# Kernel optimization log

Hardware: AMD Instinct MI355X
Metric: run time of the kernel (lower is better)

## Reference

```python
import jax, jax.numpy as jnp
import numpy as np
from jax import lax

H, W = 8192, 8192
KH, KW = 3, 3


def setup_inputs() -> dict:
    key = jax.random.key(0)
    k1, k2 = jax.random.split(key)
    x = jax.random.normal(k1, (H, W), dtype=jnp.float32)
    weight = jax.random.uniform(k2, (KH, KW), dtype=jnp.float32)
    bias = jnp.zeros((1,), dtype=jnp.float32)
    return {"x": x, "weight": weight, "bias": bias}


def reference(x, weight, bias):
    # Valid 2D cross-correlation (same math as the nested-loop corr2d) + scalar bias.
    # x: [H, W], weight: [kh, kw] -> out: [H-kh+1, W-kw+1]
    out = lax.conv_general_dilated(
        x[None, None, :, :],           # NCHW
        weight[None, None, :, :],      # OIHW
        window_strides=(1, 1),
        padding="VALID",
    )[0, 0]
    return out + bias[0]
```

## Files before the change

### kernel.cpp

```cpp
#include <hip/hip_runtime.h>


static constexpr int H  = 8192;
static constexpr int W  = 8192;
static constexpr int OH = H - 2;
static constexpr int OW = W - 2;

typedef float f32x4 __attribute__((ext_vector_type(4)));
typedef float f32x2 __attribute__((ext_vector_type(2)));

__global__ __launch_bounds__(256) void conv3x3_kernel(
    const float* __restrict__ x,
    const float* __restrict__ w,
    const float* __restrict__ bias,
    float* __restrict__ out)
{
    const int c = (blockIdx.x * 64 + (int)threadIdx.x) * 8;
    const int r = (blockIdx.y * 4 + (int)threadIdx.y) * 4;
    if (r >= OH || c >= OW) return;

    float wk[3][3];
    #pragma unroll
    for (int i = 0; i < 3; ++i)
        #pragma unroll
        for (int j = 0; j < 3; ++j)
            wk[i][j] = w[i * 3 + j];
    const float b = bias[0];

    const bool colFast = (c + 10 <= W);

    float in[6][10];
    #pragma unroll
    for (int t = 0; t < 6; ++t) {
        int rr = r + t; rr = (rr < H) ? rr : (H - 1);
        const float* row = x + (size_t)rr * W + c;
        const f32x4 va = *reinterpret_cast<const f32x4*>(row);
        const f32x4 vb = *reinterpret_cast<const f32x4*>(row + 4);
        in[t][0] = va.x; in[t][1] = va.y; in[t][2] = va.z; in[t][3] = va.w;
        in[t][4] = vb.x; in[t][5] = vb.y; in[t][6] = vb.z; in[t][7] = vb.w;
        if (colFast) {
            const f32x2 vc = *reinterpret_cast<const f32x2*>(row + 8);
            in[t][8] = vc.x; in[t][9] = vc.y;
        } else {
            in[t][8] = 0.0f; in[t][9] = 0.0f;
        }
    }

    float acc[4][8];
    #pragma unroll
    for (int i = 0; i < 4; ++i)
        #pragma unroll
        for (int j = 0; j < 8; ++j)
            acc[i][j] = b;

    #pragma unroll
    for (int i = 0; i < 4; ++i) {
        #pragma unroll
        for (int kr = 0; kr < 3; ++kr) {
            const int t = i + kr;
            const float k0 = wk[kr][0], k1 = wk[kr][1], k2 = wk[kr][2];
            #pragma unroll
            for (int j = 0; j < 8; ++j)
                acc[i][j] = fmaf(k0, in[t][j],
                            fmaf(k1, in[t][j + 1],
                            fmaf(k2, in[t][j + 2], acc[i][j])));
        }
    }

    #pragma unroll
    for (int i = 0; i < 4; ++i) {
        if (r + i < OH) {
            float* orow = out + (size_t)(r + i) * OW + c;
            if (c + 8 <= OW) {
                if ((i & 1) == 0) {
                    f32x4 o0 = { acc[i][0], acc[i][1], acc[i][2], acc[i][3] };
                    f32x4 o1 = { acc[i][4], acc[i][5], acc[i][6], acc[i][7] };
                    __builtin_nontemporal_store(o0, reinterpret_cast<f32x4*>(orow));
                    __builtin_nontemporal_store(o1, reinterpret_cast<f32x4*>(orow + 4));
                } else {
                    f32x2 o0 = { acc[i][0], acc[i][1] };
                    f32x2 o1 = { acc[i][2], acc[i][3] };
                    f32x2 o2 = { acc[i][4], acc[i][5] };
                    f32x2 o3 = { acc[i][6], acc[i][7] };
                    __builtin_nontemporal_store(o0, reinterpret_cast<f32x2*>(orow));
                    __builtin_nontemporal_store(o1, reinterpret_cast<f32x2*>(orow + 2));
                    __builtin_nontemporal_store(o2, reinterpret_cast<f32x2*>(orow + 4));
                    __builtin_nontemporal_store(o3, reinterpret_cast<f32x2*>(orow + 6));
                }
            } else {
                #pragma unroll
                for (int j = 0; j < 6; ++j)
                    __builtin_nontemporal_store(acc[i][j], orow + j);
            }
        }
    }
}

extern "C" void kernel_launch(void* const* d_in, const int* in_sizes, int n_in,
                              void* d_out, int out_size, void* d_ws, size_t ws_size,
                              hipStream_t stream) {
    const float* x    = (const float*)d_in[0];
    const float* w    = (const float*)d_in[1];
    const float* bias = (const float*)d_in[2];
    float* out        = (float*)d_out;

    dim3 block(64, 4, 1);
    dim3 grid((OW + 512 - 1) / 512,
              (OH + 16 - 1) / 16,
              1);
    conv3x3_kernel<<<grid, block, 0, stream>>>(x, w, bias, out);
}
```

Baseline: 93.18 us.

## Process eight row tiles per thread with sliding window and prefetch

Each thread now handles 32 output rows as eight 4-row tiles. It keeps the two halo rows in registers between tiles instead of reloading them, and issues the next tile's four row loads before computing the current tile. This cuts redundant input reads from 6/4 to about 34/32 per output row and gives some software pipelining. In exchange the grid shrinks eightfold (to about 1040 blocks) and register pressure rises, so occupancy and parallelism drop.

```diff
diff --git a/kernel.cpp b/kernel.cpp
--- a/kernel.cpp
+++ b/kernel.cpp
@@ -5,9 +5,28 @@
 static constexpr int W  = 8192;
 static constexpr int OH = H - 2;
 static constexpr int OW = W - 2;
+static constexpr int TILES = 8;
 
 typedef float f32x4 __attribute__((ext_vector_type(4)));
 typedef float f32x2 __attribute__((ext_vector_type(2)));
+
+__device__ __forceinline__ void loadRow(float (&dst)[10],
+                                        const float* __restrict__ x,
+                                        int rr, int c, bool colFast)
+{
+    rr = (rr < H) ? rr : (H - 1);
+    const float* row = x + (size_t)rr * W + c;
+    const f32x4 va = *reinterpret_cast<const f32x4*>(row);
+    const f32x4 vb = *reinterpret_cast<const f32x4*>(row + 4);
+    dst[0] = va.x; dst[1] = va.y; dst[2] = va.z; dst[3] = va.w;
+    dst[4] = vb.x; dst[5] = vb.y; dst[6] = vb.z; dst[7] = vb.w;
+    if (colFast) {
+        const f32x2 vc = *reinterpret_cast<const f32x2*>(row + 8);
+        dst[8] = vc.x; dst[9] = vc.y;
+    } else {
+        dst[8] = 0.0f; dst[9] = 0.0f;
+    }
+}
 
 __global__ __launch_bounds__(256) void conv3x3_kernel(
     const float* __restrict__ x,
@@ -15,9 +34,9 @@
     const float* __restrict__ bias,
     float* __restrict__ out)
 {
-    const int c = (blockIdx.x * 64 + (int)threadIdx.x) * 8;
-    const int r = (blockIdx.y * 4 + (int)threadIdx.y) * 4;
-    if (r >= OH || c >= OW) return;
+    const int c  = (blockIdx.x * 64 + (int)threadIdx.x) * 8;
+    const int r0 = (blockIdx.y * 4 + (int)threadIdx.y) * (4 * TILES);
+    if (c >= OW || r0 >= OH) return;
 
     float wk[3][3];
     #pragma unroll
@@ -29,69 +48,82 @@
 
     const bool colFast = (c + 10 <= W);
 
-    float in[6][10];
+    float cur[6][10];
     #pragma unroll
-    for (int t = 0; t < 6; ++t) {
-        int rr = r + t; rr = (rr < H) ? rr : (H - 1);
-        const float* row = x + (size_t)rr * W + c;
-        const f32x4 va = *reinterpret_cast<const f32x4*>(row);
-        const f32x4 vb = *reinterpret_cast<const f32x4*>(row + 4);
-        in[t][0] = va.x; in[t][1] = va.y; in[t][2] = va.z; in[t][3] = va.w;
-        in[t][4] = vb.x; in[t][5] = vb.y; in[t][6] = vb.z; in[t][7] = vb.w;
-        if (colFast) {
-            const f32x2 vc = *reinterpret_cast<const f32x2*>(row + 8);
-            in[t][8] = vc.x; in[t][9] = vc.y;
-        } else {
-            in[t][8] = 0.0f; in[t][9] = 0.0f;
-        }
-    }
-
-    float acc[4][8];
-    #pragma unroll
-    for (int i = 0; i < 4; ++i)
-        #pragma unroll
-        for (int j = 0; j < 8; ++j)
-            acc[i][j] = b;
+    for (int t = 0; t < 6; ++t)
+        loadRow(cur[t], x, r0 + t, c, colFast);
 
     #pragma unroll
-    for (int i = 0; i < 4; ++i) {
+    for (int it = 0; it < TILES; ++it) {
+        const int r = r0 + it * 4;
+
+        float nxt[4][10];
+        if (it + 1 < TILES) {
+            #pragma unroll
+            for (int t = 0; t < 4; ++t)
+                loadRow(nxt[t], x, r + 6 + t, c, colFast);
+        }
+
+        float acc[4][8];
         #pragma unroll
-        for (int kr = 0; kr < 3; ++kr) {
-            const int t = i + kr;
-            const float k0 = wk[kr][0], k1 = wk[kr][1], k2 = wk[kr][2];
+        for (int i = 0; i < 4; ++i)
             #pragma unroll
             for (int j = 0; j < 8; ++j)
-                acc[i][j] = fmaf(k0, in[t][j],
-                            fmaf(k1, in[t][j + 1],
-                            fmaf(k2, in[t][j + 2], acc[i][j])));
+                acc[i][j] = b;
+
+        #pragma unroll
+        for (int i = 0; i < 4; ++i) {
+            #pragma unroll
+            for (int kr = 0; kr < 3; ++kr) {
+                const int t = i + kr;
+                const float k0 = wk[kr][0], k1 = wk[kr][1], k2 = wk[kr][2];
+                #pragma unroll
+                for (int j = 0; j < 8; ++j)
+                    acc[i][j] = fmaf(k0, cur[t][j],
+                                fmaf(k1, cur[t][j + 1],
+                                fmaf(k2, cur[t][j + 2], acc[i][j])));
+            }
         }
-    }
 
-    #pragma unroll
-    for (int i = 0; i < 4; ++i) {
-        if (r + i < OH) {
-            float* orow = out + (size_t)(r + i) * OW + c;
-            if (c + 8 <= OW) {
-                if ((i & 1) == 0) {
-                    f32x4 o0 = { acc[i][0], acc[i][1], acc[i][2], acc[i][3] };
-                    f32x4 o1 = { acc[i][4], acc[i][5], acc[i][6], acc[i][7] };
-                    __builtin_nontemporal_store(o0, reinterpret_cast<f32x4*>(orow));
-                    __builtin_nontemporal_store(o1, reinterpret_cast<f32x4*>(orow + 4));
+        #pragma unroll
+        for (int i = 0; i < 4; ++i) {
+            if (r + i < OH) {
+                float* orow = out + (size_t)(r + i) * OW + c;
+                if (c + 8 <= OW) {
+                    if ((i & 1) == 0) {
+                        f32x4 o0 = { acc[i][0], acc[i][1], acc[i][2], acc[i][3] };
+                        f32x4 o1 = { acc[i][4], acc[i][5], acc[i][6], acc[i][7] };
+                        __builtin_nontemporal_store(o0, reinterpret_cast<f32x4*>(orow));
+                        __builtin_nontemporal_store(o1, reinterpret_cast<f32x4*>(orow + 4));
+                    } else {
+                        f32x2 o0 = { acc[i][0], acc[i][1] };
+                        f32x2 o1 = { acc[i][2], acc[i][3] };
+                        f32x2 o2 = { acc[i][4], acc[i][5] };
+                        f32x2 o3 = { acc[i][6], acc[i][7] };
+                        __builtin_nontemporal_store(o0, reinterpret_cast<f32x2*>(orow));
+                        __builtin_nontemporal_store(o1, reinterpret_cast<f32x2*>(orow + 2));
+                        __builtin_nontemporal_store(o2, reinterpret_cast<f32x2*>(orow + 4));
+                        __builtin_nontemporal_store(o3, reinterpret_cast<f32x2*>(orow + 6));
+                    }
                 } else {
-                    f32x2 o0 = { acc[i][0], acc[i][1] };
-                    f32x2 o1 = { acc[i][2], acc[i][3] };
-                    f32x2 o2 = { acc[i][4], acc[i][5] };
-                    f32x2 o3 = { acc[i][6], acc[i][7] };
-                    __builtin_nontemporal_store(o0, reinterpret_cast<f32x2*>(orow));
-                    __builtin_nontemporal_store(o1, reinterpret_cast<f32x2*>(orow + 2));
-                    __builtin_nontemporal_store(o2, reinterpret_cast<f32x2*>(orow + 4));
-                    __builtin_nontemporal_store(o3, reinterpret_cast<f32x2*>(orow + 6));
+                    #pragma unroll
+                    for (int j = 0; j < 6; ++j)
+                        __builtin_nontemporal_store(acc[i][j], orow + j);
                 }
-            } else {
+            }
+        }
+
+        if (it + 1 < TILES) {
+            #pragma unroll
+            for (int q = 0; q < 10; ++q) {
+                cur[0][q] = cur[4][q];
+                cur[1][q] = cur[5][q];
+            }
+            #pragma unroll
+            for (int t = 0; t < 4; ++t)
                 #pragma unroll
-                for (int j = 0; j < 6; ++j)
-                    __builtin_nontemporal_store(acc[i][j], orow + j);
-            }
+                for (int q = 0; q < 10; ++q)
+                    cur[2 + t][q] = nxt[t][q];
         }
     }
 }
@@ -106,7 +138,7 @@
 
     dim3 block(64, 4, 1);
     dim3 grid((OW + 512 - 1) / 512,
-              (OH + 16 - 1) / 16,
+              (OH + 128 - 1) / 128,
               1);
     conv3x3_kernel<<<grid, block, 0, stream>>>(x, w, bias, out);
 }
```

New measurement: 112.9 us. 21.2% more time.
